# Kernel optimization log

Measured on AMD Instinct MI355X. Metric: run time of the kernel, lower is better.

Reference implementation:

```python
import jax, jax.numpy as jnp
import numpy as np

B, S, HID = 4, 2048, 2048
NH, NKV = 8, 1
HD = HID // NH  # 256
G = NH // NKV   # queries per kv head
ROPE_THETA = 10000.0
NEG_INF = -1e9


def setup_inputs() -> dict:
    key = jax.random.key(0)
    ks = jax.random.split(key, 4)
    x = jax.random.normal(ks[0], (B, S, HID), jnp.float32)
    qkv_dim = (NH + 2 * NKV) * HD
    w_qkv = jax.random.normal(ks[1], (HID, qkv_dim), jnp.float32) * (HID ** -0.5)
    b_qkv = jnp.zeros((qkv_dim,), jnp.float32)
    w_o = jax.random.normal(ks[2], (NH * HD, HID), jnp.float32) * ((NH * HD) ** -0.5)
    b_o = jnp.zeros((HID,), jnp.float32)
    # rotary table: cos/sin of position*inv_freq, interleaved-pair convention
    inv_freq = 1.0 / (ROPE_THETA ** (jnp.arange(0, HD, 2, dtype=jnp.float32) / HD))
    ang = jnp.outer(jnp.arange(S, dtype=jnp.float32), inv_freq)  # [S, HD/2]
    freqs_cis = jnp.stack([jnp.cos(ang), jnp.sin(ang)], axis=-1)  # [S, HD/2, 2]
    causal = jnp.tril(jnp.ones((S, S), bool))
    mask = jnp.where(causal, 0.0, NEG_INF).astype(jnp.float32)[None, None]  # [1,1,S,S]
    return dict(x=x, w_qkv=w_qkv, b_qkv=b_qkv, w_o=w_o, b_o=b_o,
                freqs_cis=freqs_cis, mask=mask)


def _rope(t, cos, sin):
    # t: [B,S,H,D]; cos/sin: [1,S,1,D/2]; interleaved complex pairs
    tp = t.reshape(*t.shape[:-1], -1, 2)
    r, i = tp[..., 0], tp[..., 1]
    out = jnp.stack([r * cos - i * sin, r * sin + i * cos], axis=-1)
    return out.reshape(t.shape)


def reference(x, w_qkv, b_qkv, w_o, b_o, freqs_cis, mask):
    b, s, _ = x.shape
    qkv = x @ w_qkv + b_qkv
    q, k, v = jnp.split(qkv, [NH * HD, NH * HD + NKV * HD], axis=-1)
    q = q.reshape(b, s, NH, HD)
    k = k.reshape(b, s, NKV, HD)
    v = v.reshape(b, s, NKV, HD)
    cos = freqs_cis[..., 0][None, :, None, :]
    sin = freqs_cis[..., 1][None, :, None, :]
    q = _rope(q, cos, sin)
    k = _rope(k, cos, sin)
    # GQA: head h attends with kv group h // G (same layout as repeat_interleave)
    qh = q.transpose(0, 2, 1, 3).reshape(b, NKV, G, s, HD)  # [B,KV,G,S,D]
    kh = k.transpose(0, 2, 1, 3)                            # [B,KV,S,D]
    vh = v.transpose(0, 2, 1, 3)
    scores = jnp.einsum('bkgqd,bksd->bkgqs', qh, kh) * (HD ** -0.5)
    scores = scores + mask[:, :, None]  # broadcast over group dim
    attn = jax.nn.softmax(scores.astype(jnp.float32), axis=-1).astype(q.dtype)
    out = jnp.einsum('bkgqs,bksd->bkgqd', attn, vh)         # [B,KV,G,S,D]
    out = out.reshape(b, NH, s, HD).transpose(0, 2, 1, 3).reshape(b, s, NH * HD)
    return out @ w_o + b_o
```

## Files before the change

### kernel.cpp

```cpp
#include <hip/hip_runtime.h>
#include <hip/hip_bf16.h>

#define B_ 4
#define S_ 2048
#define HID_ 2048
#define NH_ 8
#define HD_ 256
#define QKVN 2560

typedef unsigned short u16;
typedef __attribute__((ext_vector_type(4))) float f32x4;
typedef __attribute__((ext_vector_type(16))) float f32x16;
typedef __attribute__((ext_vector_type(8))) short bf16x8;

__device__ __forceinline__ float bf2f(u16 u) {
  union { unsigned int i; float f; } v; v.i = ((unsigned int)u) << 16; return v.f;
}
__device__ __forceinline__ u16 f2bf(float f) {
  union { unsigned int i; float f; } v; v.f = f;
  unsigned int r = v.i + 0x7fffu + ((v.i >> 16) & 1u);
  return (u16)(r >> 16);
}

__global__ void cast_f32_bf16(const float* __restrict__ in, u16* __restrict__ out, int n8) {
  int i = blockIdx.x * blockDim.x + threadIdx.x;
  int stride = gridDim.x * blockDim.x;
  for (; i < n8; i += stride) {
    const float4* p = (const float4*)(in + (size_t)i * 8);
    float4 a = p[0], b = p[1];
    u16 o[8] = {f2bf(a.x), f2bf(a.y), f2bf(a.z), f2bf(a.w),
                f2bf(b.x), f2bf(b.y), f2bf(b.z), f2bf(b.w)};
    *(uint4*)(out + (size_t)i * 8) = *(const uint4*)o;
  }
}

__global__ void transpose_cast(const float* __restrict__ in, u16* __restrict__ out, int R, int C) {
  __shared__ float t[32][33];
  int c0 = blockIdx.x * 32, r0 = blockIdx.y * 32;
  int tx = threadIdx.x, ty = threadIdx.y;
#pragma unroll
  for (int i = 0; i < 4; ++i)
    t[ty + i * 8][tx] = in[(size_t)(r0 + ty + i * 8) * C + c0 + tx];
  __syncthreads();
#pragma unroll
  for (int i = 0; i < 4; ++i)
    out[(size_t)(c0 + ty + i * 8) * R + r0 + tx] = f2bf(t[tx][ty + i * 8]);
}

__global__ void transpose_bf16(const u16* __restrict__ in, u16* __restrict__ out, int R, int C) {
  __shared__ u16 t[32][33];
  in += (size_t)blockIdx.z * R * C;
  out += (size_t)blockIdx.z * R * C;
  int c0 = blockIdx.x * 32, r0 = blockIdx.y * 32;
  int tx = threadIdx.x, ty = threadIdx.y;
#pragma unroll
  for (int i = 0; i < 4; ++i)
    t[ty + i * 8][tx] = in[(size_t)(r0 + ty + i * 8) * C + c0 + tx];
  __syncthreads();
#pragma unroll
  for (int i = 0; i < 4; ++i)
    out[(size_t)(c0 + ty + i * 8) * R + r0 + tx] = t[tx][ty + i * 8];
}

template <bool OUT_F32>
__global__ __launch_bounds__(256) void gemm_bt(const u16* __restrict__ A, const u16* __restrict__ BT,
                                               const float* __restrict__ bias, void* __restrict__ Cout,
                                               int M, int N, int K) {
  __shared__ u16 As[128 * 32];
  __shared__ u16 Bs[128 * 32];
  int nwg = gridDim.x;
  int bid = (int)blockIdx.x;
  bid = (bid & 7) * (nwg >> 3) + (bid >> 3);
  int ntiles = N >> 7;
  int m0 = (bid / ntiles) << 7, n0 = (bid % ntiles) << 7;
  int tid = threadIdx.x, w = tid >> 6, lane = tid & 63;
  int wr = w >> 1, wc = w & 1;
  int l15 = lane & 15, lg = lane >> 4;
  f32x4 acc[4][4] = {};
  int crow = lane >> 2;
  int ccol = (lane & 3) * 8;
  for (int k0 = 0; k0 < K; k0 += 32) {
#pragma unroll
    for (int i = 0; i < 2; ++i) {
      int c = w * 2 + i;
      const u16* ga = A + (size_t)(m0 + c * 16 + crow) * K + k0 + ccol;
      const u16* gb = BT + (size_t)(n0 + c * 16 + crow) * K + k0 + ccol;
      __builtin_amdgcn_global_load_lds((const __attribute__((address_space(1))) void*)ga,
                                       (__attribute__((address_space(3))) void*)(As + c * 512), 16, 0, 0);
      __builtin_amdgcn_global_load_lds((const __attribute__((address_space(1))) void*)gb,
                                       (__attribute__((address_space(3))) void*)(Bs + c * 512), 16, 0, 0);
    }
    __syncthreads();
    bf16x8 af[4], bfr[4];
#pragma unroll
    for (int r = 0; r < 4; ++r)
      af[r] = *(const bf16x8*)&As[(wr * 64 + r * 16 + l15) * 32 + lg * 8];
#pragma unroll
    for (int c = 0; c < 4; ++c)
      bfr[c] = *(const bf16x8*)&Bs[(wc * 64 + c * 16 + l15) * 32 + lg * 8];
#pragma unroll
    for (int r = 0; r < 4; ++r)
#pragma unroll
      for (int c = 0; c < 4; ++c)
        acc[r][c] = __builtin_amdgcn_mfma_f32_16x16x32_bf16(af[r], bfr[c], acc[r][c], 0, 0, 0);
    __syncthreads();
  }
#pragma unroll
  for (int r = 0; r < 4; ++r) {
    int mrow = m0 + wr * 64 + r * 16 + lg * 4;
#pragma unroll
    for (int c = 0; c < 4; ++c) {
      int col = n0 + wc * 64 + c * 16 + l15;
      float bv = bias[col];
#pragma unroll
      for (int j = 0; j < 4; ++j) {
        float v = acc[r][c][j] + bv;
        if (OUT_F32)
          ((float*)Cout)[(size_t)(mrow + j) * N + col] = v;
        else
          ((u16*)Cout)[(size_t)(mrow + j) * N + col] = f2bf(v);
      }
    }
  }
}

__global__ void rope_scatter(const u16* __restrict__ qkv, const float* __restrict__ freqs,
                             u16* __restrict__ qo, u16* __restrict__ ko, u16* __restrict__ vo) {
  const int per_row = QKVN / 8;
  const int total = B_ * S_ * per_row;
  int i = blockIdx.x * blockDim.x + threadIdx.x;
  int stride = gridDim.x * blockDim.x;
  for (; i < total; i += stride) {
    int m = i / per_row;
    int n8 = (i - m * per_row) * 8;
    int b = m >> 11, s = m & 2047;
    uint4 raw = *(const uint4*)(qkv + (size_t)m * QKVN + n8);
    const u16* u = (const u16*)&raw;
    if (n8 < 2304) {
      int d = (n8 < 2048) ? (n8 & 255) : (n8 - 2048);
      float scl = (n8 < 2048) ? (0.0625f * 1.44269504f) : 1.0f;
      const float* fp = freqs + ((size_t)s * 128 + (d >> 1)) * 2;
      float4 f0 = *(const float4*)fp;
      float4 f1 = *(const float4*)(fp + 4);
      float fc[8] = {f0.x, f0.y, f0.z, f0.w, f1.x, f1.y, f1.z, f1.w};
      u16 o[8];
#pragma unroll
      for (int p = 0; p < 4; ++p) {
        float r = bf2f(u[2 * p]), im = bf2f(u[2 * p + 1]);
        float c = fc[2 * p], sn = fc[2 * p + 1];
        o[2 * p] = f2bf((r * c - im * sn) * scl);
        o[2 * p + 1] = f2bf((r * sn + im * c) * scl);
      }
      u16* dst;
      if (n8 < 2048) {
        dst = qo + (size_t)m * 2048 + n8;
      } else {
        dst = ko + (((size_t)(b * S_ + s)) << 8) + d;
      }
      *(uint4*)dst = *(const uint4*)o;
    } else {
      int d = n8 - 2304;
      u16* dst = vo + (((size_t)(b * S_ + s)) << 8) + d;
      *(uint4*)dst = raw;
    }
  }
}


#define STAGE_K(bufofs, kt)                                                                       \
  do {                                                                                            \
    const u16* _src = Kp + ((size_t)(b * S_ + (kt) * 64)) * HD_;                                  \
    _Pragma("unroll") for (int _p = 0; _p < 4; ++_p) {                                            \
      int _idx = _p * 512 + tid;                                                                  \
      int _row = _idx >> 5, _c = _idx & 31;                                                       \
      int _scol = (((_c * 16) ^ ((_row & 7) << 4)) >> 1);                                         \
      __builtin_amdgcn_global_load_lds(                                                           \
          (const __attribute__((address_space(1))) void*)(_src + (size_t)_row * HD_ + _scol),     \
          (__attribute__((address_space(3))) void*)(KsBase + (bufofs) + _idx * 8), 16, 0, 0);     \
    }                                                                                             \
  } while (0)

#define STAGE_V(bufofs, kt)                                                                       \
  do {                                                                                            \
    const u16* _src = VTp + (size_t)b * HD_ * S_ + (kt) * 64;                                     \
    _Pragma("unroll") for (int _p = 0; _p < 4; ++_p) {                                            \
      int _idx = _p * 512 + tid;                                                                  \
      int _d = _idx >> 3, _c = _idx & 7;                                                          \
      int _scol = (((_c * 16) ^ ((_d & 7) << 4)) >> 1);                                           \
      __builtin_amdgcn_global_load_lds(                                                           \
          (const __attribute__((address_space(1))) void*)(_src + (size_t)_d * S_ + _scol),        \
          (__attribute__((address_space(3))) void*)(VsBase + (bufofs) + _idx * 8), 16, 0, 0);     \
    }                                                                                             \
  } while (0)

__global__ __launch_bounds__(512, 2) void flash_attn(const u16* __restrict__ Qp, const u16* __restrict__ Kp,
                                                     const u16* __restrict__ VTp, u16* __restrict__ Op) {
  __shared__ u16 Ks[2][64 * 256];
  __shared__ u16 Vs[2][256 * 64];
  int bid = (int)blockIdx.x;
  int b = bid & 3, t = bid >> 2;
  int tid = threadIdx.x;
  int w = tid >> 6, l = tid & 63;
  int l31 = l & 31, lh = l >> 5;
  int q_local = w * 32 + l31;
  size_t qrow = (size_t)b * 16384 + (size_t)t * 256 + q_local;
  int s_g = t * 32 + (q_local >> 3);

  u16* KsBase = &Ks[0][0];
  u16* VsBase = &Vs[0][0];

  bf16x8 qf[16];
  const u16* qp = Qp + qrow * HD_ + lh * 8;
#pragma unroll
  for (int s = 0; s < 16; ++s) qf[s] = *(const bf16x8*)(qp + s * 16);

  f32x16 oacc[8] = {};
  float m_r = -3.0e38f, l_r = 0.f;
  int nkv = t / 2 + 1;

  STAGE_K(0, 0);
  STAGE_V(0, 0);
  __syncthreads();
  int cur = 0;
  for (int kt = 0; kt < nkv; ++kt) {
    if (kt + 1 < nkv) {
      STAGE_K((cur ^ 1) * 16384, kt + 1);
      STAGE_V((cur ^ 1) * 16384, kt + 1);
    }
    const char* Kb = (const char*)KsBase + cur * 32768;
    const char* Vb = (const char*)VsBase + cur * 32768;
#pragma unroll
    for (int tau = 0; tau < 2; ++tau) {
      int k0 = kt * 64 + tau * 32;
      if (k0 > t * 32 + 31) break;
      f32x16 scv = {};
      __builtin_amdgcn_s_setprio(1);
#pragma unroll
      for (int s = 0; s < 16; ++s) {
        int row = tau * 32 + l31;
        bf16x8 kf = *(const bf16x8*)(Kb + row * 512 + ((s * 32 + lh * 16) ^ ((row & 7) << 4)));
        scv = __builtin_amdgcn_mfma_f32_32x32x16_bf16(kf, qf[s], scv, 0, 0, 0);
      }
      __builtin_amdgcn_s_setprio(0);
      if (k0 + 31 > t * 32) {
#pragma unroll
        for (int j = 0; j < 16; ++j) {
          int kg = k0 + (j & 3) + 8 * (j >> 2) + 4 * lh;
          if (kg > s_g) scv[j] = -3.0e38f;
        }
      }
      float tmax = -3.0e38f;
#pragma unroll
      for (int j = 0; j < 16; ++j) tmax = fmaxf(tmax, scv[j]);
      tmax = fmaxf(tmax, __shfl_xor(tmax, 32));
      if (!__all(tmax - m_r <= 8.0f)) {
        float mnew = fmaxf(m_r, tmax);
        float sc = exp2f(m_r - mnew);
        l_r *= sc;
#pragma unroll
        for (int dt = 0; dt < 8; ++dt) oacc[dt] *= sc;
        m_r = mnew;
      }
      float ts = 0.f;
      unsigned cpk[8];
#pragma unroll
      for (int mi = 0; mi < 8; ++mi) {
        float p0 = exp2f(scv[2 * mi] - m_r);
        float p1 = exp2f(scv[2 * mi + 1] - m_r);
        ts += p0 + p1;
        cpk[mi] = ((unsigned)f2bf(p1) << 16) | f2bf(p0);
      }
      ts += __shfl_xor(ts, 32);
      l_r += ts;
      asm volatile("v_permlane32_swap_b32 %0, %1" : "+v"(cpk[0]), "+v"(cpk[2]));
      asm volatile("v_permlane32_swap_b32 %0, %1" : "+v"(cpk[1]), "+v"(cpk[3]));
      asm volatile("v_permlane32_swap_b32 %0, %1" : "+v"(cpk[4]), "+v"(cpk[6]));
      asm volatile("v_permlane32_swap_b32 %0, %1" : "+v"(cpk[5]), "+v"(cpk[7]));
      union { unsigned u[4]; bf16x8 v; } pa, pb;
      pa.u[0] = cpk[0]; pa.u[1] = cpk[1]; pa.u[2] = cpk[2]; pa.u[3] = cpk[3];
      pb.u[0] = cpk[4]; pb.u[1] = cpk[5]; pb.u[2] = cpk[6]; pb.u[3] = cpk[7];
      __builtin_amdgcn_s_setprio(1);
#pragma unroll
      for (int dt = 0; dt < 8; ++dt) {
        int d = dt * 32 + l31;
        int swz = (d & 7) << 4;
        bf16x8 va = *(const bf16x8*)(Vb + d * 128 + (((2 * tau) * 32 + lh * 16) ^ swz));
        oacc[dt] = __builtin_amdgcn_mfma_f32_32x32x16_bf16(va, pa.v, oacc[dt], 0, 0, 0);
        bf16x8 vb2 = *(const bf16x8*)(Vb + d * 128 + (((2 * tau + 1) * 32 + lh * 16) ^ swz));
        oacc[dt] = __builtin_amdgcn_mfma_f32_32x32x16_bf16(vb2, pb.v, oacc[dt], 0, 0, 0);
      }
      __builtin_amdgcn_s_setprio(0);
    }
    __syncthreads();
    cur ^= 1;
  }

  float inv = 1.0f / l_r;
  u16* ob = Op + qrow * 256;
#pragma unroll
  for (int dt = 0; dt < 8; ++dt) {
#pragma unroll
    for (int jj = 0; jj < 4; ++jj) {
      int d0 = dt * 32 + jj * 8 + 4 * lh;
      u16 o4[4];
#pragma unroll
      for (int e = 0; e < 4; ++e) o4[e] = f2bf(oacc[dt][jj * 4 + e] * inv);
      *(unsigned long long*)(ob + d0) = *(const unsigned long long*)o4;
    }
  }
}

extern "C" void kernel_launch(void* const* d_in, const int* in_sizes, int n_in,
                              void* d_out, int out_size, void* d_ws, size_t ws_size,
                              hipStream_t stream) {
  const float* x = (const float*)d_in[0];
  const float* w_qkv = (const float*)d_in[1];
  const float* b_qkv = (const float*)d_in[2];
  const float* w_o = (const float*)d_in[3];
  const float* b_o = (const float*)d_in[4];
  const float* freqs = (const float*)d_in[5];

  char* ws = (char*)d_ws;
  u16* xb    = (u16*)ws;
  u16* wqkvT = (u16*)(ws + 33554432);
  u16* woT   = (u16*)(ws + 44040192);
  u16* qkv   = (u16*)(ws + 52428800);
  u16* qall  = (u16*)(ws + 94371840);
  u16* kbuf  = (u16*)(ws + 127926272);
  u16* vbuf  = (u16*)(ws + 132120576);
  u16* vT    = xb;
  u16* attout = qkv;

  cast_f32_bf16<<<2048, 256, 0, stream>>>(x, xb, (B_ * S_ * HID_) / 8);
  transpose_cast<<<dim3(QKVN / 32, HID_ / 32), dim3(32, 8), 0, stream>>>(w_qkv, wqkvT, HID_, QKVN);
  transpose_cast<<<dim3(HID_ / 32, HID_ / 32), dim3(32, 8), 0, stream>>>(w_o, woT, HID_, HID_);
  gemm_bt<false><<<dim3(64 * 20), 256, 0, stream>>>(xb, wqkvT, b_qkv, qkv, B_ * S_, QKVN, HID_);
  rope_scatter<<<2048, 256, 0, stream>>>(qkv, freqs, qall, kbuf, vbuf);
  transpose_bf16<<<dim3(HD_ / 32, S_ / 32, B_), dim3(32, 8), 0, stream>>>(vbuf, vT, S_, HD_);
  flash_attn<<<256, 512, 0, stream>>>(qall, kbuf, vT, attout);
  gemm_bt<true><<<dim3(64 * 16), 256, 0, stream>>>(attout, woT, b_o, d_out, B_ * S_, HID_, HID_);
}
```

Measured before the change: 471.1 us.

## Split flash attention into smaller 256-thread blocks with causal load-balanced ordering

Flash attention now launches 512 blocks of 256 threads, each owning 128 query rows, instead of 256 blocks of 512 threads. Blocks are ordered so heavy causal tiles are scheduled first, with their light partners afterwards. KV tiles shrink to 32 keys. K stays double-buffered through direct global-to-LDS loads, while V is prefetched into registers and written into a single LDS buffer after use. The aim is better CU occupancy and load balance, at the cost of more iterations, more barriers and extra register pressure from the V staging.

```diff
diff --git a/kernel.cpp b/kernel.cpp
--- a/kernel.cpp
+++ b/kernel.cpp
@@ -9,6 +9,7 @@
 #define QKVN 2560
 
 typedef unsigned short u16;
+typedef unsigned long long ull;
 typedef __attribute__((ext_vector_type(4))) float f32x4;
 typedef __attribute__((ext_vector_type(16))) float f32x16;
 typedef __attribute__((ext_vector_type(8))) short bf16x8;
@@ -155,142 +156,151 @@
       if (n8 < 2048) {
         dst = qo + (size_t)m * 2048 + n8;
       } else {
-        dst = ko + (((size_t)(b * S_ + s)) << 8) + d;
+        dst = ko + (((size_t)m) << 8) + d;
       }
       *(uint4*)dst = *(const uint4*)o;
     } else {
       int d = n8 - 2304;
-      u16* dst = vo + (((size_t)(b * S_ + s)) << 8) + d;
-      *(uint4*)dst = raw;
-    }
-  }
-}
-
-
-#define STAGE_K(bufofs, kt)                                                                       \
+      *(uint4*)(vo + (((size_t)m) << 8) + d) = raw;
+    }
+  }
+}
+
+
+#define STAGE_K(dst, kt)                                                                          \
   do {                                                                                            \
-    const u16* _src = Kp + ((size_t)(b * S_ + (kt) * 64)) * HD_;                                  \
     _Pragma("unroll") for (int _p = 0; _p < 4; ++_p) {                                            \
-      int _idx = _p * 512 + tid;                                                                  \
+      int _idx = _p * 256 + tid;                                                                  \
       int _row = _idx >> 5, _c = _idx & 31;                                                       \
-      int _scol = (((_c * 16) ^ ((_row & 7) << 4)) >> 1);                                         \
-      __builtin_amdgcn_global_load_lds(                                                           \
-          (const __attribute__((address_space(1))) void*)(_src + (size_t)_row * HD_ + _scol),     \
-          (__attribute__((address_space(3))) void*)(KsBase + (bufofs) + _idx * 8), 16, 0, 0);     \
+      const u16* _src = Kg + ((size_t)(b * S_ + (kt) * 32 + _row)) * HD_ +                        \
+                        ((((_c * 16) ^ ((_row & 7) << 4))) >> 1);                                 \
+      __builtin_amdgcn_global_load_lds((const __attribute__((address_space(1))) void*)_src,       \
+                                       (__attribute__((address_space(3))) void*)((dst) + _idx * 8), 16, 0, 0); \
     }                                                                                             \
   } while (0)
 
-#define STAGE_V(bufofs, kt)                                                                       \
+#define LOAD_V(vst, kt)                                                                           \
   do {                                                                                            \
-    const u16* _src = VTp + (size_t)b * HD_ * S_ + (kt) * 64;                                     \
     _Pragma("unroll") for (int _p = 0; _p < 4; ++_p) {                                            \
-      int _idx = _p * 512 + tid;                                                                  \
-      int _d = _idx >> 3, _c = _idx & 7;                                                          \
-      int _scol = (((_c * 16) ^ ((_d & 7) << 4)) >> 1);                                           \
-      __builtin_amdgcn_global_load_lds(                                                           \
-          (const __attribute__((address_space(1))) void*)(_src + (size_t)_d * S_ + _scol),        \
-          (__attribute__((address_space(3))) void*)(VsBase + (bufofs) + _idx * 8), 16, 0, 0);     \
+      int _idx = _p * 256 + tid;                                                                  \
+      int _d = _idx >> 2, _c = _idx & 3;                                                          \
+      vst[_p] = *(const uint4*)(VTp + ((size_t)(b * 256 + _d)) * S_ + (kt) * 32 + _c * 8);        \
     }                                                                                             \
   } while (0)
 
-__global__ __launch_bounds__(512, 2) void flash_attn(const u16* __restrict__ Qp, const u16* __restrict__ Kp,
+#define WRITE_V(vst, kt)                                                                          \
+  do {                                                                                            \
+    int _hh = (kt) & 1;                                                                           \
+    _Pragma("unroll") for (int _p = 0; _p < 4; ++_p) {                                            \
+      int _idx = _p * 256 + tid;                                                                  \
+      int _d = _idx >> 2, _c = _idx & 3;                                                          \
+      *(uint4*)((char*)Vs + _d * 128 + ((_hh * 64 + _c * 16) ^ ((_d & 7) << 4))) = vst[_p];       \
+    }                                                                                             \
+  } while (0)
+
+__global__ __launch_bounds__(256, 2) void flash_attn(const u16* __restrict__ Qp, const u16* __restrict__ Kg,
                                                      const u16* __restrict__ VTp, u16* __restrict__ Op) {
-  __shared__ u16 Ks[2][64 * 256];
-  __shared__ u16 Vs[2][256 * 64];
+  __shared__ u16 Ks[2][32 * 256];
+  __shared__ u16 Vs[256 * 64];
   int bid = (int)blockIdx.x;
-  int b = bid & 3, t = bid >> 2;
+  int easy = bid >> 8;
+  int j = bid & 255;
+  int b = j >> 6, r = j & 63;
+  int t = easy ? r : (127 - r);
   int tid = threadIdx.x;
   int w = tid >> 6, l = tid & 63;
   int l31 = l & 31, lh = l >> 5;
   int q_local = w * 32 + l31;
-  size_t qrow = (size_t)b * 16384 + (size_t)t * 256 + q_local;
-  int s_g = t * 32 + (q_local >> 3);
-
-  u16* KsBase = &Ks[0][0];
-  u16* VsBase = &Vs[0][0];
+  size_t qrow = (size_t)b * 16384 + (size_t)t * 128 + q_local;
+  int s_g = t * 16 + (q_local >> 3);
 
   bf16x8 qf[16];
   const u16* qp = Qp + qrow * HD_ + lh * 8;
 #pragma unroll
-  for (int s = 0; s < 16; ++s) qf[s] = *(const bf16x8*)(qp + s * 16);
+  for (int st = 0; st < 16; ++st) qf[st] = *(const bf16x8*)(qp + st * 16);
 
   f32x16 oacc[8] = {};
   float m_r = -3.0e38f, l_r = 0.f;
-  int nkv = t / 2 + 1;
-
-  STAGE_K(0, 0);
-  STAGE_V(0, 0);
+  int nkv = (t >> 1) + 1;
+
+  {
+    uint4 vst[4];
+    STAGE_K(&Ks[0][0], 0);
+    LOAD_V(vst, 0);
+    WRITE_V(vst, 0);
+  }
   __syncthreads();
+
   int cur = 0;
   for (int kt = 0; kt < nkv; ++kt) {
-    if (kt + 1 < nkv) {
-      STAGE_K((cur ^ 1) * 16384, kt + 1);
-      STAGE_V((cur ^ 1) * 16384, kt + 1);
-    }
-    const char* Kb = (const char*)KsBase + cur * 32768;
-    const char* Vb = (const char*)VsBase + cur * 32768;
-#pragma unroll
-    for (int tau = 0; tau < 2; ++tau) {
-      int k0 = kt * 64 + tau * 32;
-      if (k0 > t * 32 + 31) break;
-      f32x16 scv = {};
-      __builtin_amdgcn_s_setprio(1);
-#pragma unroll
-      for (int s = 0; s < 16; ++s) {
-        int row = tau * 32 + l31;
-        bf16x8 kf = *(const bf16x8*)(Kb + row * 512 + ((s * 32 + lh * 16) ^ ((row & 7) << 4)));
-        scv = __builtin_amdgcn_mfma_f32_32x32x16_bf16(kf, qf[s], scv, 0, 0, 0);
+    bool more = (kt + 1 < nkv);
+    uint4 vst[4];
+    if (more) {
+      STAGE_K(&Ks[cur ^ 1][0], kt + 1);
+      LOAD_V(vst, kt + 1);
+    }
+    const char* Kb = (const char*)&Ks[cur][0];
+    int row = l31;
+    int rsw = (row & 7) << 4;
+    f32x16 scv = {};
+    __builtin_amdgcn_s_setprio(1);
+#pragma unroll
+    for (int st = 0; st < 16; ++st) {
+      bf16x8 kf = *(const bf16x8*)(Kb + row * 512 + ((st * 32 + lh * 16) ^ rsw));
+      scv = __builtin_amdgcn_mfma_f32_32x32x16_bf16(kf, qf[st], scv, 0, 0, 0);
+    }
+    __builtin_amdgcn_s_setprio(0);
+    int k0 = kt * 32;
+    if (k0 + 31 > t * 16) {
+#pragma unroll
+      for (int jj = 0; jj < 16; ++jj) {
+        int kg = k0 + (jj & 3) + 8 * (jj >> 2) + 4 * lh;
+        if (kg > s_g) scv[jj] = -3.0e38f;
       }
-      __builtin_amdgcn_s_setprio(0);
-      if (k0 + 31 > t * 32) {
-#pragma unroll
-        for (int j = 0; j < 16; ++j) {
-          int kg = k0 + (j & 3) + 8 * (j >> 2) + 4 * lh;
-          if (kg > s_g) scv[j] = -3.0e38f;
-        }
-      }
-      float tmax = -3.0e38f;
-#pragma unroll
-      for (int j = 0; j < 16; ++j) tmax = fmaxf(tmax, scv[j]);
-      tmax = fmaxf(tmax, __shfl_xor(tmax, 32));
-      if (!__all(tmax - m_r <= 8.0f)) {
-        float mnew = fmaxf(m_r, tmax);
-        float sc = exp2f(m_r - mnew);
-        l_r *= sc;
-#pragma unroll
-        for (int dt = 0; dt < 8; ++dt) oacc[dt] *= sc;
-        m_r = mnew;
-      }
-      float ts = 0.f;
-      unsigned cpk[8];
-#pragma unroll
-      for (int mi = 0; mi < 8; ++mi) {
-        float p0 = exp2f(scv[2 * mi] - m_r);
-        float p1 = exp2f(scv[2 * mi + 1] - m_r);
-        ts += p0 + p1;
-        cpk[mi] = ((unsigned)f2bf(p1) << 16) | f2bf(p0);
-      }
-      ts += __shfl_xor(ts, 32);
-      l_r += ts;
-      asm volatile("v_permlane32_swap_b32 %0, %1" : "+v"(cpk[0]), "+v"(cpk[2]));
-      asm volatile("v_permlane32_swap_b32 %0, %1" : "+v"(cpk[1]), "+v"(cpk[3]));
-      asm volatile("v_permlane32_swap_b32 %0, %1" : "+v"(cpk[4]), "+v"(cpk[6]));
-      asm volatile("v_permlane32_swap_b32 %0, %1" : "+v"(cpk[5]), "+v"(cpk[7]));
-      union { unsigned u[4]; bf16x8 v; } pa, pb;
-      pa.u[0] = cpk[0]; pa.u[1] = cpk[1]; pa.u[2] = cpk[2]; pa.u[3] = cpk[3];
-      pb.u[0] = cpk[4]; pb.u[1] = cpk[5]; pb.u[2] = cpk[6]; pb.u[3] = cpk[7];
-      __builtin_amdgcn_s_setprio(1);
-#pragma unroll
-      for (int dt = 0; dt < 8; ++dt) {
-        int d = dt * 32 + l31;
-        int swz = (d & 7) << 4;
-        bf16x8 va = *(const bf16x8*)(Vb + d * 128 + (((2 * tau) * 32 + lh * 16) ^ swz));
-        oacc[dt] = __builtin_amdgcn_mfma_f32_32x32x16_bf16(va, pa.v, oacc[dt], 0, 0, 0);
-        bf16x8 vb2 = *(const bf16x8*)(Vb + d * 128 + (((2 * tau + 1) * 32 + lh * 16) ^ swz));
-        oacc[dt] = __builtin_amdgcn_mfma_f32_32x32x16_bf16(vb2, pb.v, oacc[dt], 0, 0, 0);
-      }
-      __builtin_amdgcn_s_setprio(0);
-    }
+    }
+    float tmax = -3.0e38f;
+#pragma unroll
+    for (int jj = 0; jj < 16; ++jj) tmax = fmaxf(tmax, scv[jj]);
+    tmax = fmaxf(tmax, __shfl_xor(tmax, 32));
+    if (!__all(tmax - m_r <= 8.0f)) {
+      float mnew = fmaxf(m_r, tmax);
+      float sc = exp2f(m_r - mnew);
+      l_r *= sc;
+#pragma unroll
+      for (int dt = 0; dt < 8; ++dt) oacc[dt] *= sc;
+      m_r = mnew;
+    }
+    float ts = 0.f;
+    unsigned cpk[8];
+#pragma unroll
+    for (int mi = 0; mi < 8; ++mi) {
+      float p0 = exp2f(scv[2 * mi] - m_r);
+      float p1 = exp2f(scv[2 * mi + 1] - m_r);
+      ts += p0 + p1;
+      cpk[mi] = ((unsigned)f2bf(p1) << 16) | f2bf(p0);
+    }
+    ts += __shfl_xor(ts, 32);
+    l_r += ts;
+    asm volatile("v_permlane32_swap_b32 %0, %1" : "+v"(cpk[0]), "+v"(cpk[2]));
+    asm volatile("v_permlane32_swap_b32 %0, %1" : "+v"(cpk[1]), "+v"(cpk[3]));
+    asm volatile("v_permlane32_swap_b32 %0, %1" : "+v"(cpk[4]), "+v"(cpk[6]));
+    asm volatile("v_permlane32_swap_b32 %0, %1" : "+v"(cpk[5]), "+v"(cpk[7]));
+    union { unsigned u[4]; bf16x8 v; } pa, pb;
+    pa.u[0] = cpk[0]; pa.u[1] = cpk[1]; pa.u[2] = cpk[2]; pa.u[3] = cpk[3];
+    pb.u[0] = cpk[4]; pb.u[1] = cpk[5]; pb.u[2] = cpk[6]; pb.u[3] = cpk[7];
+    int hh = kt & 1;
+    __builtin_amdgcn_s_setprio(1);
+#pragma unroll
+    for (int dt = 0; dt < 8; ++dt) {
+      int d = dt * 32 + l31;
+      int swz = (d & 7) << 4;
+      bf16x8 va = *(const bf16x8*)((const char*)Vs + d * 128 + ((hh * 64 + lh * 16) ^ swz));
+      oacc[dt] = __builtin_amdgcn_mfma_f32_32x32x16_bf16(va, pa.v, oacc[dt], 0, 0, 0);
+      bf16x8 vb2 = *(const bf16x8*)((const char*)Vs + d * 128 + ((hh * 64 + 32 + lh * 16) ^ swz));
+      oacc[dt] = __builtin_amdgcn_mfma_f32_32x32x16_bf16(vb2, pb.v, oacc[dt], 0, 0, 0);
+    }
+    __builtin_amdgcn_s_setprio(0);
+    if (more) WRITE_V(vst, kt + 1);
     __syncthreads();
     cur ^= 1;
   }
@@ -305,7 +315,7 @@
       u16 o4[4];
 #pragma unroll
       for (int e = 0; e < 4; ++e) o4[e] = f2bf(oacc[dt][jj * 4 + e] * inv);
-      *(unsigned long long*)(ob + d0) = *(const unsigned long long*)o4;
+      *(ull*)(ob + d0) = *(const ull*)o4;
     }
   }
 }
@@ -337,6 +347,6 @@
   gemm_bt<false><<<dim3(64 * 20), 256, 0, stream>>>(xb, wqkvT, b_qkv, qkv, B_ * S_, QKVN, HID_);
   rope_scatter<<<2048, 256, 0, stream>>>(qkv, freqs, qall, kbuf, vbuf);
   transpose_bf16<<<dim3(HD_ / 32, S_ / 32, B_), dim3(32, 8), 0, stream>>>(vbuf, vT, S_, HD_);
-  flash_attn<<<256, 512, 0, stream>>>(qall, kbuf, vT, attout);
+  flash_attn<<<512, 256, 0, stream>>>(qall, kbuf, vT, attout);
   gemm_bt<true><<<dim3(64 * 16), 256, 0, stream>>>(attout, woT, b_o, d_out, B_ * S_, HID_, HID_);
 }
```

New measurement: 544.5 us. 1.16x slower.

## Split causal attention KV range across paired query tiles and merge partials

Applied to the files above, without the earlier changes.

Each attention block now handles two query tiles, t=j and t=63-j. It processes the first half of the KV range for one tile and the second half for the other, so work per block is roughly even under the causal mask. Partial outputs are written with their running max and sum, and a new combine kernel merges the two halves with softmax rescaling. This costs an extra kernel launch, a write and read of a bf16 partial buffer plus the max/sum stats, and a second bf16 rounding of the output. The path only runs when the workspace is large enough.

```diff
diff --git a/kernel.cpp b/kernel.cpp
--- a/kernel.cpp
+++ b/kernel.cpp
@@ -9,6 +9,7 @@
 #define QKVN 2560
 
 typedef unsigned short u16;
+typedef unsigned long long ull;
 typedef __attribute__((ext_vector_type(4))) float f32x4;
 typedef __attribute__((ext_vector_type(16))) float f32x16;
 typedef __attribute__((ext_vector_type(8))) short bf16x8;
@@ -155,43 +156,112 @@
       if (n8 < 2048) {
         dst = qo + (size_t)m * 2048 + n8;
       } else {
-        dst = ko + (((size_t)(b * S_ + s)) << 8) + d;
+        dst = ko + (((size_t)m) << 8) + d;
       }
       *(uint4*)dst = *(const uint4*)o;
     } else {
       int d = n8 - 2304;
-      u16* dst = vo + (((size_t)(b * S_ + s)) << 8) + d;
-      *(uint4*)dst = raw;
-    }
-  }
-}
-
+      *(uint4*)(vo + (((size_t)m) << 8) + d) = raw;
+    }
+  }
+}
 
 #define STAGE_K(bufofs, kt)                                                                       \
   do {                                                                                            \
-    const u16* _src = Kp + ((size_t)(b * S_ + (kt) * 64)) * HD_;                                  \
+    const u16* _src0 = Kp + ((size_t)(b * S_ + (kt) * 64)) * HD_;                                 \
     _Pragma("unroll") for (int _p = 0; _p < 4; ++_p) {                                            \
       int _idx = _p * 512 + tid;                                                                  \
       int _row = _idx >> 5, _c = _idx & 31;                                                       \
       int _scol = (((_c * 16) ^ ((_row & 7) << 4)) >> 1);                                         \
       __builtin_amdgcn_global_load_lds(                                                           \
-          (const __attribute__((address_space(1))) void*)(_src + (size_t)_row * HD_ + _scol),     \
+          (const __attribute__((address_space(1))) void*)(_src0 + (size_t)_row * HD_ + _scol),    \
           (__attribute__((address_space(3))) void*)(KsBase + (bufofs) + _idx * 8), 16, 0, 0);     \
     }                                                                                             \
   } while (0)
 
 #define STAGE_V(bufofs, kt)                                                                       \
   do {                                                                                            \
-    const u16* _src = VTp + (size_t)b * HD_ * S_ + (kt) * 64;                                     \
+    const u16* _src1 = VTp + (size_t)b * HD_ * S_ + (kt) * 64;                                    \
     _Pragma("unroll") for (int _p = 0; _p < 4; ++_p) {                                            \
       int _idx = _p * 512 + tid;                                                                  \
       int _d = _idx >> 3, _c = _idx & 7;                                                          \
       int _scol = (((_c * 16) ^ ((_d & 7) << 4)) >> 1);                                           \
       __builtin_amdgcn_global_load_lds(                                                           \
-          (const __attribute__((address_space(1))) void*)(_src + (size_t)_d * S_ + _scol),        \
+          (const __attribute__((address_space(1))) void*)(_src1 + (size_t)_d * S_ + _scol),       \
           (__attribute__((address_space(3))) void*)(VsBase + (bufofs) + _idx * 8), 16, 0, 0);     \
     }                                                                                             \
   } while (0)
+
+#define FLASH_SEG_BODY()                                                                          \
+  STAGE_K(0, kb);                                                                                 \
+  STAGE_V(0, kb);                                                                                 \
+  __syncthreads();                                                                                \
+  int cur = 0;                                                                                    \
+  for (int kt = kb; kt < ke; ++kt) {                                                              \
+    if (kt + 1 < ke) {                                                                            \
+      STAGE_K((cur ^ 1) * 16384, kt + 1);                                                         \
+      STAGE_V((cur ^ 1) * 16384, kt + 1);                                                         \
+    }                                                                                             \
+    const char* Kb = (const char*)KsBase + cur * 32768;                                           \
+    const char* Vb = (const char*)VsBase + cur * 32768;                                           \
+    _Pragma("unroll") for (int tau = 0; tau < 2; ++tau) {                                         \
+      int k0 = kt * 64 + tau * 32;                                                                \
+      if (k0 > t * 32 + 31) break;                                                                \
+      f32x16 scv = {};                                                                            \
+      __builtin_amdgcn_s_setprio(1);                                                              \
+      _Pragma("unroll") for (int st = 0; st < 16; ++st) {                                         \
+        int row = tau * 32 + l31;                                                                 \
+        bf16x8 kf = *(const bf16x8*)(Kb + row * 512 + ((st * 32 + lh * 16) ^ ((row & 7) << 4)));  \
+        scv = __builtin_amdgcn_mfma_f32_32x32x16_bf16(kf, qf[st], scv, 0, 0, 0);                  \
+      }                                                                                           \
+      __builtin_amdgcn_s_setprio(0);                                                              \
+      if (k0 + 31 > t * 32) {                                                                     \
+        _Pragma("unroll") for (int jj = 0; jj < 16; ++jj) {                                       \
+          int kg = k0 + (jj & 3) + 8 * (jj >> 2) + 4 * lh;                                        \
+          if (kg > s_g) scv[jj] = -3.0e38f;                                                       \
+        }                                                                                         \
+      }                                                                                           \
+      float tmax = -3.0e38f;                                                                      \
+      _Pragma("unroll") for (int jj = 0; jj < 16; ++jj) tmax = fmaxf(tmax, scv[jj]);              \
+      tmax = fmaxf(tmax, __shfl_xor(tmax, 32));                                                   \
+      if (!__all(tmax - m_r <= 8.0f)) {                                                           \
+        float mnew = fmaxf(m_r, tmax);                                                            \
+        float sc = exp2f(m_r - mnew);                                                             \
+        l_r *= sc;                                                                                \
+        _Pragma("unroll") for (int dt = 0; dt < 8; ++dt) oacc[dt] *= sc;                          \
+        m_r = mnew;                                                                               \
+      }                                                                                           \
+      float ts = 0.f;                                                                             \
+      unsigned cpk[8];                                                                            \
+      _Pragma("unroll") for (int mi = 0; mi < 8; ++mi) {                                          \
+        float p0 = exp2f(scv[2 * mi] - m_r);                                                      \
+        float p1 = exp2f(scv[2 * mi + 1] - m_r);                                                  \
+        ts += p0 + p1;                                                                            \
+        cpk[mi] = ((unsigned)f2bf(p1) << 16) | f2bf(p0);                                          \
+      }                                                                                           \
+      ts += __shfl_xor(ts, 32);                                                                   \
+      l_r += ts;                                                                                  \
+      asm volatile("v_permlane32_swap_b32 %0, %1" : "+v"(cpk[0]), "+v"(cpk[2]));                  \
+      asm volatile("v_permlane32_swap_b32 %0, %1" : "+v"(cpk[1]), "+v"(cpk[3]));                  \
+      asm volatile("v_permlane32_swap_b32 %0, %1" : "+v"(cpk[4]), "+v"(cpk[6]));                  \
+      asm volatile("v_permlane32_swap_b32 %0, %1" : "+v"(cpk[5]), "+v"(cpk[7]));                  \
+      union { unsigned u[4]; bf16x8 v; } pa, pb;                                                  \
+      pa.u[0] = cpk[0]; pa.u[1] = cpk[1]; pa.u[2] = cpk[2]; pa.u[3] = cpk[3];                     \
+      pb.u[0] = cpk[4]; pb.u[1] = cpk[5]; pb.u[2] = cpk[6]; pb.u[3] = cpk[7];                     \
+      __builtin_amdgcn_s_setprio(1);                                                              \
+      _Pragma("unroll") for (int dt = 0; dt < 8; ++dt) {                                          \
+        int d = dt * 32 + l31;                                                                    \
+        int swz = (d & 7) << 4;                                                                   \
+        bf16x8 va = *(const bf16x8*)(Vb + d * 128 + (((2 * tau) * 32 + lh * 16) ^ swz));          \
+        oacc[dt] = __builtin_amdgcn_mfma_f32_32x32x16_bf16(va, pa.v, oacc[dt], 0, 0, 0);          \
+        bf16x8 vb2 = *(const bf16x8*)(Vb + d * 128 + (((2 * tau + 1) * 32 + lh * 16) ^ swz));     \
+        oacc[dt] = __builtin_amdgcn_mfma_f32_32x32x16_bf16(vb2, pb.v, oacc[dt], 0, 0, 0);         \
+      }                                                                                           \
+      __builtin_amdgcn_s_setprio(0);                                                              \
+    }                                                                                             \
+    __syncthreads();                                                                              \
+    cur ^= 1;                                                                                     \
+  }
 
 __global__ __launch_bounds__(512, 2) void flash_attn(const u16* __restrict__ Qp, const u16* __restrict__ Kp,
                                                      const u16* __restrict__ VTp, u16* __restrict__ Op) {
@@ -205,96 +275,16 @@
   int q_local = w * 32 + l31;
   size_t qrow = (size_t)b * 16384 + (size_t)t * 256 + q_local;
   int s_g = t * 32 + (q_local >> 3);
-
   u16* KsBase = &Ks[0][0];
   u16* VsBase = &Vs[0][0];
-
   bf16x8 qf[16];
   const u16* qp = Qp + qrow * HD_ + lh * 8;
 #pragma unroll
-  for (int s = 0; s < 16; ++s) qf[s] = *(const bf16x8*)(qp + s * 16);
-
+  for (int st = 0; st < 16; ++st) qf[st] = *(const bf16x8*)(qp + st * 16);
   f32x16 oacc[8] = {};
   float m_r = -3.0e38f, l_r = 0.f;
-  int nkv = t / 2 + 1;
-
-  STAGE_K(0, 0);
-  STAGE_V(0, 0);
-  __syncthreads();
-  int cur = 0;
-  for (int kt = 0; kt < nkv; ++kt) {
-    if (kt + 1 < nkv) {
-      STAGE_K((cur ^ 1) * 16384, kt + 1);
-      STAGE_V((cur ^ 1) * 16384, kt + 1);
-    }
-    const char* Kb = (const char*)KsBase + cur * 32768;
-    const char* Vb = (const char*)VsBase + cur * 32768;
-#pragma unroll
-    for (int tau = 0; tau < 2; ++tau) {
-      int k0 = kt * 64 + tau * 32;
-      if (k0 > t * 32 + 31) break;
-      f32x16 scv = {};
-      __builtin_amdgcn_s_setprio(1);
-#pragma unroll
-      for (int s = 0; s < 16; ++s) {
-        int row = tau * 32 + l31;
-        bf16x8 kf = *(const bf16x8*)(Kb + row * 512 + ((s * 32 + lh * 16) ^ ((row & 7) << 4)));
-        scv = __builtin_amdgcn_mfma_f32_32x32x16_bf16(kf, qf[s], scv, 0, 0, 0);
-      }
-      __builtin_amdgcn_s_setprio(0);
-      if (k0 + 31 > t * 32) {
-#pragma unroll
-        for (int j = 0; j < 16; ++j) {
-          int kg = k0 + (j & 3) + 8 * (j >> 2) + 4 * lh;
-          if (kg > s_g) scv[j] = -3.0e38f;
-        }
-      }
-      float tmax = -3.0e38f;
-#pragma unroll
-      for (int j = 0; j < 16; ++j) tmax = fmaxf(tmax, scv[j]);
-      tmax = fmaxf(tmax, __shfl_xor(tmax, 32));
-      if (!__all(tmax - m_r <= 8.0f)) {
-        float mnew = fmaxf(m_r, tmax);
-        float sc = exp2f(m_r - mnew);
-        l_r *= sc;
-#pragma unroll
-        for (int dt = 0; dt < 8; ++dt) oacc[dt] *= sc;
-        m_r = mnew;
-      }
-      float ts = 0.f;
-      unsigned cpk[8];
-#pragma unroll
-      for (int mi = 0; mi < 8; ++mi) {
-        float p0 = exp2f(scv[2 * mi] - m_r);
-        float p1 = exp2f(scv[2 * mi + 1] - m_r);
-        ts += p0 + p1;
-        cpk[mi] = ((unsigned)f2bf(p1) << 16) | f2bf(p0);
-      }
-      ts += __shfl_xor(ts, 32);
-      l_r += ts;
-      asm volatile("v_permlane32_swap_b32 %0, %1" : "+v"(cpk[0]), "+v"(cpk[2]));
-      asm volatile("v_permlane32_swap_b32 %0, %1" : "+v"(cpk[1]), "+v"(cpk[3]));
-      asm volatile("v_permlane32_swap_b32 %0, %1" : "+v"(cpk[4]), "+v"(cpk[6]));
-      asm volatile("v_permlane32_swap_b32 %0, %1" : "+v"(cpk[5]), "+v"(cpk[7]));
-      union { unsigned u[4]; bf16x8 v; } pa, pb;
-      pa.u[0] = cpk[0]; pa.u[1] = cpk[1]; pa.u[2] = cpk[2]; pa.u[3] = cpk[3];
-      pb.u[0] = cpk[4]; pb.u[1] = cpk[5]; pb.u[2] = cpk[6]; pb.u[3] = cpk[7];
-      __builtin_amdgcn_s_setprio(1);
-#pragma unroll
-      for (int dt = 0; dt < 8; ++dt) {
-        int d = dt * 32 + l31;
-        int swz = (d & 7) << 4;
-        bf16x8 va = *(const bf16x8*)(Vb + d * 128 + (((2 * tau) * 32 + lh * 16) ^ swz));
-        oacc[dt] = __builtin_amdgcn_mfma_f32_32x32x16_bf16(va, pa.v, oacc[dt], 0, 0, 0);
-        bf16x8 vb2 = *(const bf16x8*)(Vb + d * 128 + (((2 * tau + 1) * 32 + lh * 16) ^ swz));
-        oacc[dt] = __builtin_amdgcn_mfma_f32_32x32x16_bf16(vb2, pb.v, oacc[dt], 0, 0, 0);
-      }
-      __builtin_amdgcn_s_setprio(0);
-    }
-    __syncthreads();
-    cur ^= 1;
-  }
-
+  int kb = 0, ke = t / 2 + 1;
+  FLASH_SEG_BODY();
   float inv = 1.0f / l_r;
   u16* ob = Op + qrow * 256;
 #pragma unroll
@@ -305,8 +295,85 @@
       u16 o4[4];
 #pragma unroll
       for (int e = 0; e < 4; ++e) o4[e] = f2bf(oacc[dt][jj * 4 + e] * inv);
-      *(unsigned long long*)(ob + d0) = *(const unsigned long long*)o4;
-    }
+      *(ull*)(ob + d0) = *(const ull*)o4;
+    }
+  }
+}
+
+__global__ __launch_bounds__(512, 2) void flash_attn_split(const u16* __restrict__ Qp, const u16* __restrict__ Kp,
+                                                           const u16* __restrict__ VTp, u16* __restrict__ P0,
+                                                           float* __restrict__ ml0, float* __restrict__ ml1,
+                                                           u16* __restrict__ Op) {
+  __shared__ u16 Ks[2][64 * 256];
+  __shared__ u16 Vs[2][256 * 64];
+  int bid = (int)blockIdx.x;
+  int b = (bid & 7) >> 1;
+  int j = ((bid & 1) << 5) + (bid >> 3);
+  int tid = threadIdx.x;
+  int w = tid >> 6, l = tid & 63;
+  int l31 = l & 31, lh = l >> 5;
+  int q_local = w * 32 + l31;
+  u16* KsBase = &Ks[0][0];
+  u16* VsBase = &Vs[0][0];
+
+  for (int seg = 0; seg < 2; ++seg) {
+    int t = seg ? (63 - j) : j;
+    int nkv = (t >> 1) + 1;
+    int half = (nkv + 1) >> 1;
+    int kb = seg ? half : 0;
+    int ke = seg ? nkv : half;
+    size_t qrow = (size_t)b * 16384 + (size_t)t * 256 + q_local;
+    int s_g = t * 32 + (q_local >> 3);
+    float* mlbuf = seg ? ml1 : ml0;
+    if (kb >= ke) {
+      if (lh == 0) { mlbuf[qrow * 2] = -3.0e38f; mlbuf[qrow * 2 + 1] = 0.f; }
+      continue;
+    }
+    bf16x8 qf[16];
+    const u16* qp = Qp + qrow * HD_ + lh * 8;
+#pragma unroll
+    for (int st = 0; st < 16; ++st) qf[st] = *(const bf16x8*)(qp + st * 16);
+    f32x16 oacc[8] = {};
+    float m_r = -3.0e38f, l_r = 0.f;
+    FLASH_SEG_BODY();
+    float inv = 1.0f / l_r;
+    u16* ob = (seg ? Op : P0) + qrow * 256;
+#pragma unroll
+    for (int dt = 0; dt < 8; ++dt) {
+#pragma unroll
+      for (int jj = 0; jj < 4; ++jj) {
+        int d0 = dt * 32 + jj * 8 + 4 * lh;
+        u16 o4[4];
+#pragma unroll
+        for (int e = 0; e < 4; ++e) o4[e] = f2bf(oacc[dt][jj * 4 + e] * inv);
+        *(ull*)(ob + d0) = *(const ull*)o4;
+      }
+    }
+    if (lh == 0) { mlbuf[qrow * 2] = m_r; mlbuf[qrow * 2 + 1] = l_r; }
+  }
+}
+
+__global__ __launch_bounds__(256) void combine_parts(const u16* __restrict__ P0, const float* __restrict__ ml0,
+                                                     const float* __restrict__ ml1, u16* __restrict__ O) {
+  int r = blockIdx.x * 256 + threadIdx.x;
+  float m0 = ml0[(size_t)r * 2], l0 = ml0[(size_t)r * 2 + 1];
+  float m1 = ml1[(size_t)r * 2], l1 = ml1[(size_t)r * 2 + 1];
+  float M = fmaxf(m0, m1);
+  float w0 = l0 * exp2f(m0 - M), w1 = l1 * exp2f(m1 - M);
+  float inv = 1.0f / (w0 + w1);
+  w0 *= inv; w1 *= inv;
+  const u16* p0 = P0 + (size_t)r * 256;
+  u16* p1 = O + (size_t)r * 256;
+#pragma unroll 4
+  for (int c = 0; c < 32; ++c) {
+    uint4 a = *(const uint4*)(p0 + c * 8);
+    uint4 bq = *(const uint4*)(p1 + c * 8);
+    const u16* ua = (const u16*)&a;
+    const u16* ub = (const u16*)&bq;
+    u16 o[8];
+#pragma unroll
+    for (int e = 0; e < 8; ++e) o[e] = f2bf(w0 * bf2f(ua[e]) + w1 * bf2f(ub[e]));
+    *(uint4*)(p1 + c * 8) = *(const uint4*)o;
   }
 }
 
@@ -328,8 +395,13 @@
   u16* qall  = (u16*)(ws + 94371840);
   u16* kbuf  = (u16*)(ws + 127926272);
   u16* vbuf  = (u16*)(ws + 132120576);
+  u16* part0 = (u16*)(ws + 136314880);
+  float* ml0 = (float*)(ws + 169869312);
+  float* ml1 = (float*)(ws + 170393600);
   u16* vT    = xb;
   u16* attout = qkv;
+
+  bool split = (ws_size >= 170917888ULL);
 
   cast_f32_bf16<<<2048, 256, 0, stream>>>(x, xb, (B_ * S_ * HID_) / 8);
   transpose_cast<<<dim3(QKVN / 32, HID_ / 32), dim3(32, 8), 0, stream>>>(w_qkv, wqkvT, HID_, QKVN);
@@ -337,6 +409,11 @@
   gemm_bt<false><<<dim3(64 * 20), 256, 0, stream>>>(xb, wqkvT, b_qkv, qkv, B_ * S_, QKVN, HID_);
   rope_scatter<<<2048, 256, 0, stream>>>(qkv, freqs, qall, kbuf, vbuf);
   transpose_bf16<<<dim3(HD_ / 32, S_ / 32, B_), dim3(32, 8), 0, stream>>>(vbuf, vT, S_, HD_);
-  flash_attn<<<256, 512, 0, stream>>>(qall, kbuf, vT, attout);
+  if (split) {
+    flash_attn_split<<<256, 512, 0, stream>>>(qall, kbuf, vT, part0, ml0, ml1, attout);
+    combine_parts<<<256, 256, 0, stream>>>(part0, ml0, ml1, attout);
+  } else {
+    flash_attn<<<256, 512, 0, stream>>>(qall, kbuf, vT, attout);
+  }
   gemm_bt<true><<<dim3(64 * 16), 256, 0, stream>>>(attout, woT, b_o, d_out, B_ * S_, HID_, HID_);
 }
```

Result: slower. 483.1 us (+2.5%).
